# Optimization experiments

Measured on AMD Instinct MI355X. Metric: run time of the kernel, lower is better.

The kernel has to match this reference:

```python
import jax, jax.numpy as jnp
import numpy as np

B, S, D = 8, 1024, 512


def setup_inputs() -> dict:
    key = jax.random.key(0)
    k1, k2, k3, k4, k5, k6, k7 = jax.random.split(key, 7)
    inp = jax.random.normal(k1, (B, S, D), dtype=jnp.float32)
    aspect = jax.random.normal(k2, (B, S, D), dtype=jnp.float32)
    # lengths in [S//2, S], with max exactly S (the module requires max(len)==S)
    inp_len = jax.random.randint(k3, (B,), S // 2, S + 1).astype(jnp.float32)
    inp_len = inp_len.at[0].set(float(S))
    lim = float(np.sqrt(6.0 / (D + D)))  # xavier_uniform bound
    w1 = jax.random.uniform(k4, (D, D), jnp.float32, -lim, lim)
    b1 = jax.random.uniform(k5, (D,), jnp.float32, -lim, lim)
    w2 = jax.random.uniform(k6, (D, D), jnp.float32, -lim, lim)
    b2 = jax.random.uniform(k7, (D,), jnp.float32, -lim, lim)
    return {"inp": inp, "inp_len": inp_len, "aspect": aspect,
            "w1": w1, "b1": b1, "w2": w2, "b2": b2}


def reference(inp, inp_len, aspect, w1, b1, w2, b2):
    # inp, aspect: [B,S,D]; inp_len: [B] float lengths with max == S
    Bv, Sv, Dv = inp.shape
    scale = jnp.sqrt(inp_len)[:, None, None]                      # [B,1,1]
    att = jnp.einsum('bsd,btd->bst', aspect, inp) / scale          # [B,S,S]
    # mask over the query (row) dimension, as in the original expand
    mask = (jnp.arange(Sv)[None, :] < inp_len.astype(jnp.int32)[:, None]).astype(inp.dtype)  # [B,S]
    exp = att * mask[:, :, None]
    att_n = exp / (jnp.sum(exp, axis=-1, keepdims=True) + 1e-4)    # linear (non-exp) normalize
    weighted = jnp.einsum('bst,btd->bsd', att_n, inp)              # [B,S,D]
    ffn_inp = weighted + (inp + aspect) * mask[:, :, None]
    # FFN: two square linears with relu, plus inner residual
    o1 = jax.nn.relu(jnp.einsum('bsd,ed->bse', ffn_inp, w1) + b1)
    o2 = jax.nn.relu(jnp.einsum('bsd,ed->bse', o1, w2) + b2)
    ffn_out = o2 + ffn_inp
    final = ffn_inp + ffn_out
    return final / jnp.linalg.norm(final, axis=2, keepdims=True)
```

## Files before the change

### kernel.cpp

```cpp
#include <hip/hip_runtime.h>

#define Bq 8
#define Sq 1024
#define Dq 512

typedef __attribute__((ext_vector_type(8))) short bf16x8;
typedef __attribute__((ext_vector_type(4))) float f32x4;

__device__ __forceinline__ unsigned short f2bf(float f) {
  unsigned int u = __float_as_uint(f);
  return (unsigned short)((u + 0x7fffu + ((u >> 16) & 1u)) >> 16);
}
__device__ __forceinline__ float bf2f(unsigned short h) {
  return __uint_as_float(((unsigned int)h) << 16);
}

__device__ __forceinline__ void load_lds16(const unsigned short* g, unsigned short* l) {
  __builtin_amdgcn_global_load_lds(
      (const __attribute__((address_space(1))) unsigned int*)g,
      (__attribute__((address_space(3))) unsigned int*)l, 16, 0, 0);
}

__global__ void convert_w(const float* __restrict__ w1, unsigned short* __restrict__ w1b,
                          const float* __restrict__ w2, unsigned short* __restrict__ w2b) {
  int blk = blockIdx.x;
  const float* src = (blk < 256) ? w1 : w2;
  unsigned short* dst = (blk < 256) ? w1b : w2b;
  int i = ((blk & 255) * 256 + threadIdx.x) * 4;
  float4 v = *(const float4*)(src + i);
  ushort4 o;
  o.x = f2bf(v.x); o.y = f2bf(v.y); o.z = f2bf(v.z); o.w = f2bf(v.w);
  *(ushort4*)(dst + i) = o;
}

__global__ void prep_inp(const float* __restrict__ inp, unsigned short* __restrict__ inp_bf,
                         unsigned short* __restrict__ inpT, float* __restrict__ colsum) {
  __shared__ unsigned short tile[32][33];
  __shared__ float csum[8][33];
  int b = blockIdx.x;
  int t0 = blockIdx.y * 32, d0 = blockIdx.z * 32;
  int tx = threadIdx.x, ty = threadIdx.y;
  const float* src = inp + ((size_t)b * Sq + t0) * Dq + d0;
  unsigned short* dbf = inp_bf + ((size_t)b * Sq + t0) * Dq + d0;
  float part = 0.f;
#pragma unroll
  for (int i = 0; i < 4; ++i) {
    float v = src[(size_t)(ty + i * 8) * Dq + tx];
    unsigned short h = f2bf(v);
    tile[ty + i * 8][tx] = h;
    dbf[(size_t)(ty + i * 8) * Dq + tx] = h;
    part += v;
  }
  csum[ty][tx] = part;
  __syncthreads();
  unsigned short* dst = inpT + (size_t)b * Dq * Sq;
#pragma unroll
  for (int i = 0; i < 4; ++i)
    dst[(size_t)(d0 + ty + i * 8) * Sq + t0 + tx] = tile[tx][ty + i * 8];
  if (ty == 0) {
    float s = 0.f;
#pragma unroll
    for (int i = 0; i < 8; ++i) s += csum[i][tx];
    atomicAdd(&colsum[b * Dq + d0 + tx], s);
  }
}

__global__ void prep_asp(const float* __restrict__ aspect, const float* __restrict__ colsum,
                         const float* __restrict__ lenv, unsigned short* __restrict__ asp_bf,
                         float* __restrict__ fac) {
  int row = blockIdx.x * 4 + (threadIdx.x >> 6);
  int lane = threadIdx.x & 63;
  int b = row >> 10, s = row & 1023;
  const float* a = aspect + (size_t)row * Dq + lane * 8;
  const float* c = colsum + b * Dq + lane * 8;
  float4 a0 = *(const float4*)a, a1 = *(const float4*)(a + 4);
  float4 c0 = *(const float4*)c, c1 = *(const float4*)(c + 4);
  float sum = a0.x * c0.x + a0.y * c0.y + a0.z * c0.z + a0.w * c0.w +
              a1.x * c1.x + a1.y * c1.y + a1.z * c1.z + a1.w * c1.w;
  ushort4 o0; o0.x = f2bf(a0.x); o0.y = f2bf(a0.y); o0.z = f2bf(a0.z); o0.w = f2bf(a0.w);
  ushort4 o1; o1.x = f2bf(a1.x); o1.y = f2bf(a1.y); o1.z = f2bf(a1.z); o1.w = f2bf(a1.w);
  unsigned short* dst = asp_bf + (size_t)row * Dq + lane * 8;
  *(ushort4*)dst = o0;
  *(ushort4*)(dst + 4) = o1;
#pragma unroll
  for (int o = 32; o; o >>= 1) sum += __shfl_xor(sum, o, 64);
  if (lane == 0) {
    float len = lenv[b];
    float scale = sqrtf(len);
    float f = 0.f;
    if (s < (int)len) f = 1.f / (scale * (sum / scale + 1e-4f));
    fac[row] = f;
  }
}

struct EpiArgs {
  const float* fac;
  const unsigned short* inpb;
  const unsigned short* aspb;
  const float* lenv;
  const float* bias;
  const float* resid;
  float* outF;
  unsigned short* outBf;
};

template <int EPI, int MODE, int K>
__global__ __launch_bounds__(256, 5) void gemm_bf16(
    const unsigned short* __restrict__ Ag, const unsigned short* __restrict__ Bg,
    int M, int N, long strideA, long strideB, long strideOF, long strideOBf,
    EpiArgs e) {
  __shared__ unsigned short sA[2][64 * 64];
  __shared__ unsigned short sB[2][64 * 64];
  int b, bm, bn;
  if (MODE == 0) { b = blockIdx.x; bm = blockIdx.y; bn = blockIdx.z; }
  else           { b = 0; bm = blockIdx.x; bn = blockIdx.y; }
  const unsigned short* Ab = Ag + (size_t)b * strideA + (size_t)bm * 64 * K;
  const unsigned short* Bb = Bg + (size_t)b * strideB + (size_t)bn * 64 * K;
  int tid = threadIdx.x;
  int lane = tid & 63, wave = tid >> 6;
  int wm = (wave >> 1) * 32, wn = (wave & 1) * 32;
  int lr = lane & 15, lq = lane >> 4;
  int x7 = lr & 7;
  int l3 = lane >> 3, l7 = lane & 7;

  int r0 = wave * 16;
  const unsigned short* gA = Ab + (size_t)(r0 + l3) * K + (l7 ^ l3) * 8;
  const unsigned short* gB = Bb + (size_t)(r0 + l3) * K + (l7 ^ l3) * 8;
  int dbase0 = (r0 * 8 + lane) * 8;
  int dbase1 = ((r0 + 8) * 8 + lane) * 8;

  f32x4 acc[2][2] = {};

  auto issue = [&](int buf, int k0) {
    load_lds16(gA + k0, &sA[buf][dbase0]);
    load_lds16(gA + (size_t)8 * K + k0, &sA[buf][dbase1]);
    load_lds16(gB + k0, &sB[buf][dbase0]);
    load_lds16(gB + (size_t)8 * K + k0, &sB[buf][dbase1]);
  };

  const int nk = K >> 6;
  issue(0, 0);
#pragma unroll
  for (int it = 0; it < nk; ++it) {
    int cur = it & 1;
    __syncthreads();
    if (it + 1 < nk) issue(cur ^ 1, (it + 1) << 6);
#pragma unroll
    for (int c = 0; c < 2; ++c) {
      int g = c * 4 + lq;
      bf16x8 a0 = *(const bf16x8*)&sA[cur][((wm + lr) * 8 + (g ^ x7)) * 8];
      bf16x8 a1 = *(const bf16x8*)&sA[cur][((wm + 16 + lr) * 8 + (g ^ x7)) * 8];
      bf16x8 b0 = *(const bf16x8*)&sB[cur][((wn + lr) * 8 + (g ^ x7)) * 8];
      bf16x8 b1 = *(const bf16x8*)&sB[cur][((wn + 16 + lr) * 8 + (g ^ x7)) * 8];
      acc[0][0] = __builtin_amdgcn_mfma_f32_16x16x32_bf16(a0, b0, acc[0][0], 0, 0, 0);
      acc[0][1] = __builtin_amdgcn_mfma_f32_16x16x32_bf16(a0, b1, acc[0][1], 0, 0, 0);
      acc[1][0] = __builtin_amdgcn_mfma_f32_16x16x32_bf16(a1, b0, acc[1][0], 0, 0, 0);
      acc[1][1] = __builtin_amdgcn_mfma_f32_16x16x32_bf16(a1, b1, acc[1][1], 0, 0, 0);
    }
  }

#pragma unroll
  for (int mi = 0; mi < 2; ++mi) {
#pragma unroll
    for (int ni = 0; ni < 2; ++ni) {
#pragma unroll
      for (int i = 0; i < 4; ++i) {
        int r = bm * 64 + wm + mi * 16 + lq * 4 + i;
        int cc = bn * 64 + wn + ni * 16 + lr;
        float v = acc[mi][ni][i];
        if (EPI == 0) {
          e.outBf[(size_t)b * strideOBf + (size_t)r * N + cc] = f2bf(v);
        } else if (EPI == 2) {
          float f = e.fac[(size_t)b * M + r];
          int len = (int)e.lenv[b];
          size_t idx = (size_t)b * ((size_t)Sq * Dq) + (size_t)r * Dq + cc;
          float add = (r < len) ? (bf2f(e.inpb[idx]) + bf2f(e.aspb[idx])) : 0.f;
          float o = v * f + add;
          e.outF[(size_t)b * strideOF + (size_t)r * N + cc] = o;
          e.outBf[(size_t)b * strideOBf + (size_t)r * N + cc] = f2bf(o);
        } else if (EPI == 3) {
          float o = fmaxf(v + e.bias[cc], 0.f);
          e.outBf[(size_t)r * N + cc] = f2bf(o);
        } else {
          float o = fmaxf(v + e.bias[cc], 0.f);
          size_t idx = (size_t)r * N + cc;
          e.outF[idx] = 2.f * e.resid[idx] + o;
        }
      }
    }
  }
}

__global__ void norm_kernel(const float* __restrict__ fin, float* __restrict__ out) {
  int row = blockIdx.x * 4 + (threadIdx.x >> 6);
  int lane = threadIdx.x & 63;
  const float* p = fin + (size_t)row * Dq;
  float4 v0 = *(const float4*)(p + lane * 8);
  float4 v1 = *(const float4*)(p + lane * 8 + 4);
  float ss = v0.x * v0.x + v0.y * v0.y + v0.z * v0.z + v0.w * v0.w +
             v1.x * v1.x + v1.y * v1.y + v1.z * v1.z + v1.w * v1.w;
#pragma unroll
  for (int o = 32; o; o >>= 1) ss += __shfl_xor(ss, o, 64);
  float rn = 1.f / sqrtf(ss);
  float* q = out + (size_t)row * Dq;
  v0.x *= rn; v0.y *= rn; v0.z *= rn; v0.w *= rn;
  v1.x *= rn; v1.y *= rn; v1.z *= rn; v1.w *= rn;
  *(float4*)(q + lane * 8) = v0;
  *(float4*)(q + lane * 8 + 4) = v1;
}

extern "C" void kernel_launch(void* const* d_in, const int* in_sizes, int n_in,
                              void* d_out, int out_size, void* d_ws, size_t ws_size,
                              hipStream_t stream) {
  const float* inp = (const float*)d_in[0];
  const float* inp_len = (const float*)d_in[1];
  const float* aspect = (const float*)d_in[2];
  const float* w1 = (const float*)d_in[3];
  const float* b1 = (const float*)d_in[4];
  const float* w2 = (const float*)d_in[5];
  const float* b2 = (const float*)d_in[6];
  float* out = (float*)d_out;

  char* W = (char*)d_ws;
  const size_t MB = 1ull << 20;
  unsigned short* inp_bf = (unsigned short*)(W + 0);
  unsigned short* asp_bf = (unsigned short*)(W + 8 * MB);
  unsigned short* inpT   = (unsigned short*)(W + 16 * MB);
  unsigned short* Gm     = (unsigned short*)(W + 24 * MB);
  float*          finalF = (float*)(W + 16 * MB);
  float*          ffnF   = (float*)(W + 32 * MB);
  unsigned short* ffnBf  = (unsigned short*)(W + 48 * MB);
  unsigned short* o1b    = (unsigned short*)(W + 56 * MB);
  unsigned short* w1bf   = (unsigned short*)(W + 64 * MB);
  unsigned short* w2bf   = (unsigned short*)(W + 64 * MB + 512 * 1024);
  float*          colsum = (float*)(W + 65 * MB);
  float*          fac    = (float*)(W + 65 * MB + 64 * 1024);

  hipMemsetAsync(colsum, 0, Bq * Dq * sizeof(float), stream);
  prep_inp<<<dim3(8, 32, 16), dim3(32, 8), 0, stream>>>(inp, inp_bf, inpT, colsum);
  convert_w<<<512, 256, 0, stream>>>(w1, w1bf, w2, w2bf);
  prep_asp<<<2048, 256, 0, stream>>>(aspect, colsum, inp_len, asp_bf, fac);

  {
    EpiArgs e{};
    e.outBf = Gm;
    gemm_bf16<0, 0, 1024><<<dim3(8, 8, 8), 256, 0, stream>>>(
        inpT, inpT, 512, 512,
        (long)Dq * Sq, (long)Dq * Sq, 0, (long)Dq * Dq, e);
  }
  {
    EpiArgs e{};
    e.fac = fac; e.inpb = inp_bf; e.aspb = asp_bf; e.lenv = inp_len;
    e.outF = ffnF; e.outBf = ffnBf;
    gemm_bf16<2, 0, 512><<<dim3(8, 16, 8), 256, 0, stream>>>(
        asp_bf, Gm, 1024, 512,
        (long)Sq * Dq, (long)Dq * Dq, (long)Sq * Dq, (long)Sq * Dq, e);
  }
  {
    EpiArgs e{};
    e.bias = b1; e.outBf = o1b;
    gemm_bf16<3, 1, 512><<<dim3(128, 8), 256, 0, stream>>>(
        ffnBf, w1bf, 8192, 512, 0, 0, 0, 0, e);
  }
  {
    EpiArgs e{};
    e.bias = b2; e.resid = ffnF; e.outF = finalF;
    gemm_bf16<4, 1, 512><<<dim3(128, 8), 256, 0, stream>>>(
        o1b, w2bf, 8192, 512, 0, 0, 0, 0, e);
  }
  norm_kernel<<<2048, 256, 0, stream>>>(finalF, out);
}
```

Measured before the change: 158.0 us.

## Fuse attention-apply, two FFN GEMMs and row normalization into one kernel

```diff
diff --git a/kernel.cpp b/kernel.cpp
--- a/kernel.cpp
+++ b/kernel.cpp
@@ -93,29 +93,14 @@
   }
 }
 
-struct EpiArgs {
-  const float* fac;
-  const unsigned short* inpb;
-  const unsigned short* aspb;
-  const float* lenv;
-  const float* bias;
-  const float* resid;
-  float* outF;
-  unsigned short* outBf;
-};
-
-template <int EPI, int MODE, int K>
-__global__ __launch_bounds__(256, 5) void gemm_bf16(
-    const unsigned short* __restrict__ Ag, const unsigned short* __restrict__ Bg,
-    int M, int N, long strideA, long strideB, long strideOF, long strideOBf,
-    EpiArgs e) {
+__global__ __launch_bounds__(256, 5) void gemm_gram(
+    const unsigned short* __restrict__ Ag, int K, long strideA, long strideO,
+    unsigned short* __restrict__ outBf) {
   __shared__ unsigned short sA[2][64 * 64];
   __shared__ unsigned short sB[2][64 * 64];
-  int b, bm, bn;
-  if (MODE == 0) { b = blockIdx.x; bm = blockIdx.y; bn = blockIdx.z; }
-  else           { b = 0; bm = blockIdx.x; bn = blockIdx.y; }
+  int b = blockIdx.x, bm = blockIdx.y, bn = blockIdx.z;
   const unsigned short* Ab = Ag + (size_t)b * strideA + (size_t)bm * 64 * K;
-  const unsigned short* Bb = Bg + (size_t)b * strideB + (size_t)bn * 64 * K;
+  const unsigned short* Bb = Ag + (size_t)b * strideA + (size_t)bn * 64 * K;
   int tid = threadIdx.x;
   int lane = tid & 63, wave = tid >> 6;
   int wm = (wave >> 1) * 32, wn = (wave & 1) * 32;
@@ -160,53 +145,150 @@
   }
 
 #pragma unroll
-  for (int mi = 0; mi < 2; ++mi) {
-#pragma unroll
-    for (int ni = 0; ni < 2; ++ni) {
+  for (int mi = 0; mi < 2; ++mi)
+#pragma unroll
+    for (int ni = 0; ni < 2; ++ni)
 #pragma unroll
       for (int i = 0; i < 4; ++i) {
         int r = bm * 64 + wm + mi * 16 + lq * 4 + i;
         int cc = bn * 64 + wn + ni * 16 + lr;
-        float v = acc[mi][ni][i];
-        if (EPI == 0) {
-          e.outBf[(size_t)b * strideOBf + (size_t)r * N + cc] = f2bf(v);
-        } else if (EPI == 2) {
-          float f = e.fac[(size_t)b * M + r];
-          int len = (int)e.lenv[b];
-          size_t idx = (size_t)b * ((size_t)Sq * Dq) + (size_t)r * Dq + cc;
-          float add = (r < len) ? (bf2f(e.inpb[idx]) + bf2f(e.aspb[idx])) : 0.f;
-          float o = v * f + add;
-          e.outF[(size_t)b * strideOF + (size_t)r * N + cc] = o;
-          e.outBf[(size_t)b * strideOBf + (size_t)r * N + cc] = f2bf(o);
-        } else if (EPI == 3) {
-          float o = fmaxf(v + e.bias[cc], 0.f);
-          e.outBf[(size_t)r * N + cc] = f2bf(o);
-        } else {
-          float o = fmaxf(v + e.bias[cc], 0.f);
-          size_t idx = (size_t)r * N + cc;
-          e.outF[idx] = 2.f * e.resid[idx] + o;
-        }
+        outBf[(size_t)b * strideO + (size_t)r * 512 + cc] = f2bf(acc[mi][ni][i]);
       }
+}
+
+#define LP 520
+
+__global__ __launch_bounds__(512, 2) void mega_ffn(
+    const unsigned short* __restrict__ aspb, const unsigned short* __restrict__ G,
+    const unsigned short* __restrict__ w1b, const unsigned short* __restrict__ w2b,
+    const float* __restrict__ b1, const float* __restrict__ b2,
+    const float* __restrict__ inp, const float* __restrict__ aspect,
+    const float* __restrict__ fac, const float* __restrict__ lenv,
+    float* __restrict__ out) {
+  __shared__ unsigned short ldsA[32 * LP];
+  __shared__ float ssqW[2][4][16];
+  int tid = threadIdx.x;
+  int lane = tid & 63, wave = tid >> 6;
+  int mg = wave >> 2, ng = wave & 3;
+  int lr = lane & 15, lq = lane >> 4;
+  int r0 = blockIdx.x * 32;
+  int b = r0 >> 10;
+  int c0 = ng * 128;
+  int arow = r0 + mg * 16 + lr;
+
+  bf16x8 af[16];
+  f32x4 acc[8];
+  f32x4 ffnv[8];
+
+#pragma unroll
+  for (int j = 0; j < 16; ++j)
+    af[j] = *(const bf16x8*)(aspb + (size_t)arow * 512 + j * 32 + lq * 8);
+#pragma unroll
+  for (int t = 0; t < 8; ++t) acc[t] = (f32x4){0.f, 0.f, 0.f, 0.f};
+  const unsigned short* Gb = G + (size_t)b * 512 * 512;
+#pragma unroll
+  for (int j = 0; j < 16; ++j) {
+    bf16x8 bfr[8];
+#pragma unroll
+    for (int t = 0; t < 8; ++t)
+      bfr[t] = *(const bf16x8*)(Gb + (size_t)(c0 + t * 16 + lr) * 512 + j * 32 + lq * 8);
+#pragma unroll
+    for (int t = 0; t < 8; ++t)
+      acc[t] = __builtin_amdgcn_mfma_f32_16x16x32_bf16(af[j], bfr[t], acc[t], 0, 0, 0);
+  }
+  int len = (int)lenv[b];
+  float facv[4];
+#pragma unroll
+  for (int i = 0; i < 4; ++i) facv[i] = fac[r0 + mg * 16 + lq * 4 + i];
+#pragma unroll
+  for (int t = 0; t < 8; ++t) {
+#pragma unroll
+    for (int i = 0; i < 4; ++i) {
+      int r = r0 + mg * 16 + lq * 4 + i;
+      size_t idx = (size_t)r * 512 + c0 + t * 16 + lr;
+      float add = ((r & 1023) < len) ? (inp[idx] + aspect[idx]) : 0.f;
+      float v = acc[t][i] * facv[i] + add;
+      ffnv[t][i] = v;
+      ldsA[(mg * 16 + lq * 4 + i) * LP + c0 + t * 16 + lr] = f2bf(v);
     }
   }
-}
-
-__global__ void norm_kernel(const float* __restrict__ fin, float* __restrict__ out) {
-  int row = blockIdx.x * 4 + (threadIdx.x >> 6);
-  int lane = threadIdx.x & 63;
-  const float* p = fin + (size_t)row * Dq;
-  float4 v0 = *(const float4*)(p + lane * 8);
-  float4 v1 = *(const float4*)(p + lane * 8 + 4);
-  float ss = v0.x * v0.x + v0.y * v0.y + v0.z * v0.z + v0.w * v0.w +
-             v1.x * v1.x + v1.y * v1.y + v1.z * v1.z + v1.w * v1.w;
-#pragma unroll
-  for (int o = 32; o; o >>= 1) ss += __shfl_xor(ss, o, 64);
-  float rn = 1.f / sqrtf(ss);
-  float* q = out + (size_t)row * Dq;
-  v0.x *= rn; v0.y *= rn; v0.z *= rn; v0.w *= rn;
-  v1.x *= rn; v1.y *= rn; v1.z *= rn; v1.w *= rn;
-  *(float4*)(q + lane * 8) = v0;
-  *(float4*)(q + lane * 8 + 4) = v1;
+  __syncthreads();
+
+#pragma unroll
+  for (int j = 0; j < 16; ++j)
+    af[j] = *(const bf16x8*)&ldsA[(mg * 16 + lr) * LP + j * 32 + lq * 8];
+  __syncthreads();
+#pragma unroll
+  for (int t = 0; t < 8; ++t) acc[t] = (f32x4){0.f, 0.f, 0.f, 0.f};
+#pragma unroll
+  for (int j = 0; j < 16; ++j) {
+    bf16x8 bfr[8];
+#pragma unroll
+    for (int t = 0; t < 8; ++t)
+      bfr[t] = *(const bf16x8*)(w1b + (size_t)(c0 + t * 16 + lr) * 512 + j * 32 + lq * 8);
+#pragma unroll
+    for (int t = 0; t < 8; ++t)
+      acc[t] = __builtin_amdgcn_mfma_f32_16x16x32_bf16(af[j], bfr[t], acc[t], 0, 0, 0);
+  }
+  float biasv[8];
+#pragma unroll
+  for (int t = 0; t < 8; ++t) biasv[t] = b1[c0 + t * 16 + lr];
+#pragma unroll
+  for (int t = 0; t < 8; ++t)
+#pragma unroll
+    for (int i = 0; i < 4; ++i)
+      ldsA[(mg * 16 + lq * 4 + i) * LP + c0 + t * 16 + lr] =
+          f2bf(fmaxf(acc[t][i] + biasv[t], 0.f));
+  __syncthreads();
+
+#pragma unroll
+  for (int j = 0; j < 16; ++j)
+    af[j] = *(const bf16x8*)&ldsA[(mg * 16 + lr) * LP + j * 32 + lq * 8];
+#pragma unroll
+  for (int t = 0; t < 8; ++t) acc[t] = (f32x4){0.f, 0.f, 0.f, 0.f};
+#pragma unroll
+  for (int j = 0; j < 16; ++j) {
+    bf16x8 bfr[8];
+#pragma unroll
+    for (int t = 0; t < 8; ++t)
+      bfr[t] = *(const bf16x8*)(w2b + (size_t)(c0 + t * 16 + lr) * 512 + j * 32 + lq * 8);
+#pragma unroll
+    for (int t = 0; t < 8; ++t)
+      acc[t] = __builtin_amdgcn_mfma_f32_16x16x32_bf16(af[j], bfr[t], acc[t], 0, 0, 0);
+  }
+#pragma unroll
+  for (int t = 0; t < 8; ++t) biasv[t] = b2[c0 + t * 16 + lr];
+  float ssq[4] = {0.f, 0.f, 0.f, 0.f};
+#pragma unroll
+  for (int t = 0; t < 8; ++t)
+#pragma unroll
+    for (int i = 0; i < 4; ++i) {
+      float v = 2.f * ffnv[t][i] + fmaxf(acc[t][i] + biasv[t], 0.f);
+      ffnv[t][i] = v;
+      ssq[i] += v * v;
+    }
+#pragma unroll
+  for (int off = 1; off < 16; off <<= 1)
+#pragma unroll
+    for (int i = 0; i < 4; ++i) ssq[i] += __shfl_xor(ssq[i], off, 64);
+  if (lr == 0)
+#pragma unroll
+    for (int i = 0; i < 4; ++i) ssqW[mg][ng][lq * 4 + i] = ssq[i];
+  __syncthreads();
+  float rn[4];
+#pragma unroll
+  for (int i = 0; i < 4; ++i) {
+    float s = ssqW[mg][0][lq * 4 + i] + ssqW[mg][1][lq * 4 + i] +
+              ssqW[mg][2][lq * 4 + i] + ssqW[mg][3][lq * 4 + i];
+    rn[i] = 1.f / sqrtf(s);
+  }
+#pragma unroll
+  for (int t = 0; t < 8; ++t)
+#pragma unroll
+    for (int i = 0; i < 4; ++i) {
+      int r = r0 + mg * 16 + lq * 4 + i;
+      out[(size_t)r * 512 + c0 + t * 16 + lr] = ffnv[t][i] * rn[i];
+    }
 }
 
 extern "C" void kernel_launch(void* const* d_in, const int* in_sizes, int n_in,
@@ -227,46 +309,19 @@
   unsigned short* asp_bf = (unsigned short*)(W + 8 * MB);
   unsigned short* inpT   = (unsigned short*)(W + 16 * MB);
   unsigned short* Gm     = (unsigned short*)(W + 24 * MB);
-  float*          finalF = (float*)(W + 16 * MB);
-  float*          ffnF   = (float*)(W + 32 * MB);
-  unsigned short* ffnBf  = (unsigned short*)(W + 48 * MB);
-  unsigned short* o1b    = (unsigned short*)(W + 56 * MB);
-  unsigned short* w1bf   = (unsigned short*)(W + 64 * MB);
-  unsigned short* w2bf   = (unsigned short*)(W + 64 * MB + 512 * 1024);
-  float*          colsum = (float*)(W + 65 * MB);
-  float*          fac    = (float*)(W + 65 * MB + 64 * 1024);
+  unsigned short* w1bf   = (unsigned short*)(W + 28 * MB);
+  unsigned short* w2bf   = (unsigned short*)(W + 28 * MB + 512 * 1024);
+  float*          colsum = (float*)(W + 29 * MB);
+  float*          fac    = (float*)(W + 29 * MB + 64 * 1024);
 
   hipMemsetAsync(colsum, 0, Bq * Dq * sizeof(float), stream);
   prep_inp<<<dim3(8, 32, 16), dim3(32, 8), 0, stream>>>(inp, inp_bf, inpT, colsum);
   convert_w<<<512, 256, 0, stream>>>(w1, w1bf, w2, w2bf);
   prep_asp<<<2048, 256, 0, stream>>>(aspect, colsum, inp_len, asp_bf, fac);
 
-  {
-    EpiArgs e{};
-    e.outBf = Gm;
-    gemm_bf16<0, 0, 1024><<<dim3(8, 8, 8), 256, 0, stream>>>(
-        inpT, inpT, 512, 512,
-        (long)Dq * Sq, (long)Dq * Sq, 0, (long)Dq * Dq, e);
-  }
-  {
-    EpiArgs e{};
-    e.fac = fac; e.inpb = inp_bf; e.aspb = asp_bf; e.lenv = inp_len;
-    e.outF = ffnF; e.outBf = ffnBf;
-    gemm_bf16<2, 0, 512><<<dim3(8, 16, 8), 256, 0, stream>>>(
-        asp_bf, Gm, 1024, 512,
-        (long)Sq * Dq, (long)Dq * Dq, (long)Sq * Dq, (long)Sq * Dq, e);
-  }
-  {
-    EpiArgs e{};
-    e.bias = b1; e.outBf = o1b;
-    gemm_bf16<3, 1, 512><<<dim3(128, 8), 256, 0, stream>>>(
-        ffnBf, w1bf, 8192, 512, 0, 0, 0, 0, e);
-  }
-  {
-    EpiArgs e{};
-    e.bias = b2; e.resid = ffnF; e.outF = finalF;
-    gemm_bf16<4, 1, 512><<<dim3(128, 8), 256, 0, stream>>>(
-        o1b, w2bf, 8192, 512, 0, 0, 0, 0, e);
-  }
-  norm_kernel<<<2048, 256, 0, stream>>>(finalF, out);
-}
+  gemm_gram<<<dim3(8, 8, 8), 256, 0, stream>>>(
+      inpT, 1024, (long)Dq * Sq, (long)Dq * Dq, Gm);
+
+  mega_ffn<<<256, 512, 0, stream>>>(
+      asp_bf, Gm, w1bf, w2bf, b1, b2, inp, aspect, fac, inp_len, out);
+}
```

Measured after the change: 213.7 us. +35.3%, slower.

## Exploit Gram symmetry, drop atomics and bf16 inp copy, fuse weight conversion

Applied to the files above, without the earlier changes.

```diff
diff --git a/kernel.cpp b/kernel.cpp
--- a/kernel.cpp
+++ b/kernel.cpp
@@ -10,9 +10,6 @@
 __device__ __forceinline__ unsigned short f2bf(float f) {
   unsigned int u = __float_as_uint(f);
   return (unsigned short)((u + 0x7fffu + ((u >> 16) & 1u)) >> 16);
-}
-__device__ __forceinline__ float bf2f(unsigned short h) {
-  return __uint_as_float(((unsigned int)h) << 16);
 }
 
 __device__ __forceinline__ void load_lds16(const unsigned short* g, unsigned short* l) {
@@ -21,34 +18,19 @@
       (__attribute__((address_space(3))) unsigned int*)l, 16, 0, 0);
 }
 
-__global__ void convert_w(const float* __restrict__ w1, unsigned short* __restrict__ w1b,
-                          const float* __restrict__ w2, unsigned short* __restrict__ w2b) {
-  int blk = blockIdx.x;
-  const float* src = (blk < 256) ? w1 : w2;
-  unsigned short* dst = (blk < 256) ? w1b : w2b;
-  int i = ((blk & 255) * 256 + threadIdx.x) * 4;
-  float4 v = *(const float4*)(src + i);
-  ushort4 o;
-  o.x = f2bf(v.x); o.y = f2bf(v.y); o.z = f2bf(v.z); o.w = f2bf(v.w);
-  *(ushort4*)(dst + i) = o;
-}
-
-__global__ void prep_inp(const float* __restrict__ inp, unsigned short* __restrict__ inp_bf,
-                         unsigned short* __restrict__ inpT, float* __restrict__ colsum) {
+__global__ void prep_inp(const float* __restrict__ inp, unsigned short* __restrict__ inpT,
+                         float* __restrict__ partial) {
   __shared__ unsigned short tile[32][33];
   __shared__ float csum[8][33];
   int b = blockIdx.x;
   int t0 = blockIdx.y * 32, d0 = blockIdx.z * 32;
   int tx = threadIdx.x, ty = threadIdx.y;
   const float* src = inp + ((size_t)b * Sq + t0) * Dq + d0;
-  unsigned short* dbf = inp_bf + ((size_t)b * Sq + t0) * Dq + d0;
   float part = 0.f;
 #pragma unroll
   for (int i = 0; i < 4; ++i) {
     float v = src[(size_t)(ty + i * 8) * Dq + tx];
-    unsigned short h = f2bf(v);
-    tile[ty + i * 8][tx] = h;
-    dbf[(size_t)(ty + i * 8) * Dq + tx] = h;
+    tile[ty + i * 8][tx] = f2bf(v);
     part += v;
   }
   csum[ty][tx] = part;
@@ -61,42 +43,137 @@
     float s = 0.f;
 #pragma unroll
     for (int i = 0; i < 8; ++i) s += csum[i][tx];
-    atomicAdd(&colsum[b * Dq + d0 + tx], s);
-  }
-}
-
-__global__ void prep_asp(const float* __restrict__ aspect, const float* __restrict__ colsum,
-                         const float* __restrict__ lenv, unsigned short* __restrict__ asp_bf,
-                         float* __restrict__ fac) {
-  int row = blockIdx.x * 4 + (threadIdx.x >> 6);
-  int lane = threadIdx.x & 63;
-  int b = row >> 10, s = row & 1023;
-  const float* a = aspect + (size_t)row * Dq + lane * 8;
-  const float* c = colsum + b * Dq + lane * 8;
-  float4 a0 = *(const float4*)a, a1 = *(const float4*)(a + 4);
-  float4 c0 = *(const float4*)c, c1 = *(const float4*)(c + 4);
-  float sum = a0.x * c0.x + a0.y * c0.y + a0.z * c0.z + a0.w * c0.w +
-              a1.x * c1.x + a1.y * c1.y + a1.z * c1.z + a1.w * c1.w;
-  ushort4 o0; o0.x = f2bf(a0.x); o0.y = f2bf(a0.y); o0.z = f2bf(a0.z); o0.w = f2bf(a0.w);
-  ushort4 o1; o1.x = f2bf(a1.x); o1.y = f2bf(a1.y); o1.z = f2bf(a1.z); o1.w = f2bf(a1.w);
-  unsigned short* dst = asp_bf + (size_t)row * Dq + lane * 8;
-  *(ushort4*)dst = o0;
-  *(ushort4*)(dst + 4) = o1;
-#pragma unroll
-  for (int o = 32; o; o >>= 1) sum += __shfl_xor(sum, o, 64);
-  if (lane == 0) {
+    partial[((size_t)b * 32 + blockIdx.y) * Dq + d0 + tx] = s;
+  }
+}
+
+__global__ __launch_bounds__(256) void prep_asp(
+    const float* __restrict__ aspect, const float* __restrict__ partial,
+    const float* __restrict__ lenv, unsigned short* __restrict__ asp_bf,
+    float* __restrict__ fac,
+    const float* __restrict__ w1, unsigned short* __restrict__ w1b,
+    const float* __restrict__ w2, unsigned short* __restrict__ w2b) {
+  int bx = blockIdx.x;
+  if (bx >= 512) {
+    int blk = bx - 512;
+    const float* src = (blk < 256) ? w1 : w2;
+    unsigned short* dst = (blk < 256) ? w1b : w2b;
+    int i = ((blk & 255) * 256 + threadIdx.x) * 4;
+    float4 v = *(const float4*)(src + i);
+    ushort4 o; o.x = f2bf(v.x); o.y = f2bf(v.y); o.z = f2bf(v.z); o.w = f2bf(v.w);
+    *(ushort4*)(dst + i) = o;
+    return;
+  }
+  __shared__ float cs[512];
+  int b = bx >> 6;
+  int s0 = (bx & 63) * 16;
+  int tid = threadIdx.x;
+#pragma unroll
+  for (int h = 0; h < 2; ++h) {
+    int d = h * 256 + tid;
+    float s = 0.f;
+    const float* p = partial + (size_t)b * 32 * Dq + d;
+#pragma unroll
+    for (int t = 0; t < 32; ++t) s += p[t * Dq];
+    cs[d] = s;
+  }
+  __syncthreads();
+  int lane = tid & 63, wave = tid >> 6;
+  int g = lane >> 4, lr = lane & 15;
+  int row = s0 + wave * 4 + g;
+  const float* a = aspect + ((size_t)b * Sq + row) * Dq + lr * 32;
+  unsigned short* dst = asp_bf + ((size_t)b * Sq + row) * Dq + lr * 32;
+  float sum = 0.f;
+#pragma unroll
+  for (int j = 0; j < 8; ++j) {
+    float4 v = *(const float4*)(a + j * 4);
+    ushort4 o; o.x = f2bf(v.x); o.y = f2bf(v.y); o.z = f2bf(v.z); o.w = f2bf(v.w);
+    *(ushort4*)(dst + j * 4) = o;
+    const float* c = cs + lr * 32 + j * 4;
+    sum += v.x * c[0] + v.y * c[1] + v.z * c[2] + v.w * c[3];
+  }
+#pragma unroll
+  for (int off = 1; off < 16; off <<= 1) sum += __shfl_xor(sum, off, 64);
+  if (lr == 0) {
     float len = lenv[b];
     float scale = sqrtf(len);
     float f = 0.f;
-    if (s < (int)len) f = 1.f / (scale * (sum / scale + 1e-4f));
-    fac[row] = f;
-  }
+    if (row < (int)len) f = 1.f / (scale * (sum / scale + 1e-4f));
+    fac[b * Sq + row] = f;
+  }
+}
+
+__global__ __launch_bounds__(256, 5) void gemm_gram(
+    const unsigned short* __restrict__ Ag, int K, long strideA, long strideO,
+    unsigned short* __restrict__ outBf) {
+  int b = blockIdx.x, bm = blockIdx.y, bn = blockIdx.z;
+  if (bn < bm) return;
+  __shared__ unsigned short sA[2][64 * 64];
+  __shared__ unsigned short sB[2][64 * 64];
+  const unsigned short* Ab = Ag + (size_t)b * strideA + (size_t)bm * 64 * K;
+  const unsigned short* Bb = Ag + (size_t)b * strideA + (size_t)bn * 64 * K;
+  int tid = threadIdx.x;
+  int lane = tid & 63, wave = tid >> 6;
+  int wm = (wave >> 1) * 32, wn = (wave & 1) * 32;
+  int lr = lane & 15, lq = lane >> 4;
+  int x7 = lr & 7;
+  int l3 = lane >> 3, l7 = lane & 7;
+
+  int r0 = wave * 16;
+  const unsigned short* gA = Ab + (size_t)(r0 + l3) * K + (l7 ^ l3) * 8;
+  const unsigned short* gB = Bb + (size_t)(r0 + l3) * K + (l7 ^ l3) * 8;
+  int dbase0 = (r0 * 8 + lane) * 8;
+  int dbase1 = ((r0 + 8) * 8 + lane) * 8;
+
+  f32x4 acc[2][2] = {};
+
+  auto issue = [&](int buf, int k0) {
+    load_lds16(gA + k0, &sA[buf][dbase0]);
+    load_lds16(gA + (size_t)8 * K + k0, &sA[buf][dbase1]);
+    load_lds16(gB + k0, &sB[buf][dbase0]);
+    load_lds16(gB + (size_t)8 * K + k0, &sB[buf][dbase1]);
+  };
+
+  const int nk = K >> 6;
+  issue(0, 0);
+#pragma unroll
+  for (int it = 0; it < nk; ++it) {
+    int cur = it & 1;
+    __syncthreads();
+    if (it + 1 < nk) issue(cur ^ 1, (it + 1) << 6);
+#pragma unroll
+    for (int c = 0; c < 2; ++c) {
+      int g = c * 4 + lq;
+      bf16x8 a0 = *(const bf16x8*)&sA[cur][((wm + lr) * 8 + (g ^ x7)) * 8];
+      bf16x8 a1 = *(const bf16x8*)&sA[cur][((wm + 16 + lr) * 8 + (g ^ x7)) * 8];
+      bf16x8 b0 = *(const bf16x8*)&sB[cur][((wn + lr) * 8 + (g ^ x7)) * 8];
+      bf16x8 b1 = *(const bf16x8*)&sB[cur][((wn + 16 + lr) * 8 + (g ^ x7)) * 8];
+      acc[0][0] = __builtin_amdgcn_mfma_f32_16x16x32_bf16(a0, b0, acc[0][0], 0, 0, 0);
+      acc[0][1] = __builtin_amdgcn_mfma_f32_16x16x32_bf16(a0, b1, acc[0][1], 0, 0, 0);
+      acc[1][0] = __builtin_amdgcn_mfma_f32_16x16x32_bf16(a1, b0, acc[1][0], 0, 0, 0);
+      acc[1][1] = __builtin_amdgcn_mfma_f32_16x16x32_bf16(a1, b1, acc[1][1], 0, 0, 0);
+    }
+  }
+
+  unsigned short* Ob = outBf + (size_t)b * strideO;
+#pragma unroll
+  for (int mi = 0; mi < 2; ++mi)
+#pragma unroll
+    for (int ni = 0; ni < 2; ++ni)
+#pragma unroll
+      for (int i = 0; i < 4; ++i) {
+        int r = bm * 64 + wm + mi * 16 + lq * 4 + i;
+        int cc = bn * 64 + wn + ni * 16 + lr;
+        unsigned short h = f2bf(acc[mi][ni][i]);
+        Ob[(size_t)r * 512 + cc] = h;
+        if (bn > bm) Ob[(size_t)cc * 512 + r] = h;
+      }
 }
 
 struct EpiArgs {
   const float* fac;
-  const unsigned short* inpb;
-  const unsigned short* aspb;
+  const float* inp;
+  const float* aspect;
   const float* lenv;
   const float* bias;
   const float* resid;
@@ -168,13 +245,11 @@
         int r = bm * 64 + wm + mi * 16 + lq * 4 + i;
         int cc = bn * 64 + wn + ni * 16 + lr;
         float v = acc[mi][ni][i];
-        if (EPI == 0) {
-          e.outBf[(size_t)b * strideOBf + (size_t)r * N + cc] = f2bf(v);
-        } else if (EPI == 2) {
+        if (EPI == 2) {
           float f = e.fac[(size_t)b * M + r];
           int len = (int)e.lenv[b];
           size_t idx = (size_t)b * ((size_t)Sq * Dq) + (size_t)r * Dq + cc;
-          float add = (r < len) ? (bf2f(e.inpb[idx]) + bf2f(e.aspb[idx])) : 0.f;
+          float add = (r < len) ? (e.inp[idx] + e.aspect[idx]) : 0.f;
           float o = v * f + add;
           e.outF[(size_t)b * strideOF + (size_t)r * N + cc] = o;
           e.outBf[(size_t)b * strideOBf + (size_t)r * N + cc] = f2bf(o);
@@ -223,34 +298,29 @@
 
   char* W = (char*)d_ws;
   const size_t MB = 1ull << 20;
-  unsigned short* inp_bf = (unsigned short*)(W + 0);
-  unsigned short* asp_bf = (unsigned short*)(W + 8 * MB);
-  unsigned short* inpT   = (unsigned short*)(W + 16 * MB);
-  unsigned short* Gm     = (unsigned short*)(W + 24 * MB);
-  float*          finalF = (float*)(W + 16 * MB);
-  float*          ffnF   = (float*)(W + 32 * MB);
-  unsigned short* ffnBf  = (unsigned short*)(W + 48 * MB);
-  unsigned short* o1b    = (unsigned short*)(W + 56 * MB);
-  unsigned short* w1bf   = (unsigned short*)(W + 64 * MB);
-  unsigned short* w2bf   = (unsigned short*)(W + 64 * MB + 512 * 1024);
-  float*          colsum = (float*)(W + 65 * MB);
-  float*          fac    = (float*)(W + 65 * MB + 64 * 1024);
-
-  hipMemsetAsync(colsum, 0, Bq * Dq * sizeof(float), stream);
-  prep_inp<<<dim3(8, 32, 16), dim3(32, 8), 0, stream>>>(inp, inp_bf, inpT, colsum);
-  convert_w<<<512, 256, 0, stream>>>(w1, w1bf, w2, w2bf);
-  prep_asp<<<2048, 256, 0, stream>>>(aspect, colsum, inp_len, asp_bf, fac);
+  unsigned short* asp_bf = (unsigned short*)(W + 0);
+  unsigned short* inpT   = (unsigned short*)(W + 8 * MB);
+  unsigned short* Gm     = (unsigned short*)(W + 16 * MB);
+  unsigned short* w1bf   = (unsigned short*)(W + 20 * MB);
+  unsigned short* w2bf   = (unsigned short*)(W + 20 * MB + 512 * 1024);
+  float*          partial= (float*)(W + 21 * MB);
+  float*          fac    = (float*)(W + 22 * MB);
+  float*          ffnF   = (float*)(W + 24 * MB);
+  unsigned short* ffnBf  = (unsigned short*)(W + 40 * MB);
+  unsigned short* o1b    = (unsigned short*)(W + 48 * MB);
+  float*          finalF = (float*)(W + 56 * MB);
+
+  prep_inp<<<dim3(8, 32, 16), dim3(32, 8), 0, stream>>>(inp, inpT, partial);
+
+  prep_asp<<<1024, 256, 0, stream>>>(aspect, partial, inp_len, asp_bf, fac,
+                                     w1, w1bf, w2, w2bf);
+
+  gemm_gram<<<dim3(8, 8, 8), 256, 0, stream>>>(
+      inpT, 1024, (long)Dq * Sq, (long)Dq * Dq, Gm);
 
   {
     EpiArgs e{};
-    e.outBf = Gm;
-    gemm_bf16<0, 0, 1024><<<dim3(8, 8, 8), 256, 0, stream>>>(
-        inpT, inpT, 512, 512,
-        (long)Dq * Sq, (long)Dq * Sq, 0, (long)Dq * Dq, e);
-  }
-  {
-    EpiArgs e{};
-    e.fac = fac; e.inpb = inp_bf; e.aspb = asp_bf; e.lenv = inp_len;
+    e.fac = fac; e.inp = inp; e.aspect = aspect; e.lenv = inp_len;
     e.outF = ffnF; e.outBf = ffnBf;
     gemm_bf16<2, 0, 512><<<dim3(8, 16, 8), 256, 0, stream>>>(
         asp_bf, Gm, 1024, 512,
```

Result: no change. 160.9 us (+1.8%).
